# Performance work log

Hardware: AMD Instinct MI355X
Metric: run time of the kernel (lower is better)

## Reference

```python
import jax, jax.numpy as jnp
import numpy as np


def _hardswish(x):
    return x * jnp.clip(x + 3.0, 0.0, 6.0) / 6.0


def _rel_coords_table(W):
    # [1, 2W-1, 2W-1, 2], log-spaced continuous relative coords (SwinV2)
    rc = jnp.arange(-(W - 1), W, dtype=jnp.float32)
    grid = jnp.stack(jnp.meshgrid(rc, rc, indexing='ij'), axis=-1)[None]
    grid = grid / float(W - 1) * 8.0
    return jnp.sign(grid) * jnp.log2(jnp.abs(grid) + 1.0) / np.float32(np.log2(8.0))


def _rel_pos_index(W):
    # [N, N] int indices into the (2W-1)^2 bias table
    coords = np.stack(np.meshgrid(np.arange(W), np.arange(W), indexing='ij')).reshape(2, -1)
    rel = (coords[:, :, None] - coords[:, None, :]).transpose(1, 2, 0)  # [N, N, 2]
    rel[:, :, 0] += W - 1
    rel[:, :, 1] += W - 1
    rel[:, :, 0] *= 2 * W - 1
    return jnp.asarray(rel.sum(-1))


def setup_inputs() -> dict:
    key = jax.random.key(0)
    ks = jax.random.split(key, 6)
    dim, num_heads, W = 512, 16, 8
    N = W * W
    B, nW = 2048, 64
    return {
        'x': jax.random.normal(ks[0], (B, N, dim), jnp.float32),
        'mask': jax.random.normal(ks[1], (nW, N, N), jnp.float32),
        'w_qkv': jax.random.normal(ks[2], (dim, 3 * dim), jnp.float32) * 0.02,
        'w_out': jax.random.normal(ks[3], (dim, dim), jnp.float32) * 0.02,
        'cpb_w1': jax.random.normal(ks[4], (2, 512), jnp.float32) * 0.02,
        'cpb_w2': jax.random.normal(ks[5], (512, num_heads), jnp.float32) * 0.02,
        'logits_scale': jnp.log(10.0 * jnp.ones((num_heads, 1, 1), jnp.float32)),
        'window_size': W,
        'num_heads': num_heads,
    }


def reference(x, mask, w_qkv, w_out, cpb_w1, cpb_w2, logits_scale, window_size, num_heads):
    B, N, C = x.shape
    hd = C // num_heads
    qkv = (x @ w_qkv).reshape(B, N, 3, num_heads, hd).transpose(2, 0, 3, 1, 4)
    q, k, v = qkv[0], qkv[1], qkv[2]  # [B, H, N, hd]

    # cosine attention (L2-normalized q, k) with clamped learned logit scale
    qn = q / jnp.clip(jnp.linalg.norm(q, axis=-1, keepdims=True), 1e-12)
    kn = k / jnp.clip(jnp.linalg.norm(k, axis=-1, keepdims=True), 1e-12)
    attn = jnp.einsum('bhnd,bhmd->bhnm', qn, kn)
    scale = jnp.exp(jnp.minimum(logits_scale, jnp.log(jnp.float32(100.0))))  # [H,1,1]
    attn = attn * scale[None]

    # continuous position bias via tiny MLP + index gather, sigmoid-scaled
    table = _rel_coords_table(window_size)                       # [1, 2W-1, 2W-1, 2]
    bias_table = (_hardswish(table @ cpb_w1) @ cpb_w2).reshape(-1, num_heads)
    idx = _rel_pos_index(window_size)                            # [N, N]
    bias = bias_table[idx.reshape(-1)].reshape(N, N, num_heads).transpose(2, 0, 1)
    attn = attn + 16.0 * jax.nn.sigmoid(bias)[None]

    if mask is not None:
        nW = mask.shape[0]
        attn = attn.reshape(B // nW, nW, num_heads, N, N) + mask[None, :, None]
        attn = attn.reshape(B, num_heads, N, N)

    # NOTE: original uses nn.Softmax(1) -> softmax over the HEAD axis; replicate faithfully
    attn = jax.nn.softmax(attn, axis=1)

    out = jnp.einsum('bhnm,bhmd->bhnd', attn, v).transpose(0, 2, 1, 3).reshape(B, N, C)
    return out @ w_out
```

## Files before the change

kernel.cpp:

```cpp
#include <hip/hip_runtime.h>
#include <hip/hip_bf16.h>

typedef unsigned short u16;
typedef unsigned int u32;
typedef __attribute__((ext_vector_type(8))) short bf16x8;
typedef __attribute__((ext_vector_type(4))) short bf16x4;
typedef __attribute__((ext_vector_type(4))) float f32x4;
typedef __attribute__((ext_vector_type(4))) float float4v;

__device__ __forceinline__ float bf2f(u16 v) {
  union { u32 u; float f; } x; x.u = ((u32)v) << 16; return x.f;
}
__device__ __forceinline__ u16 f2bf(float f) {
  union { u32 u; float f; } x; x.f = f;
  return (u16)((x.u + 0x7fffu + ((x.u >> 16) & 1u)) >> 16);
}

__device__ __forceinline__ void gload16(const void* g, void* l) {
  __builtin_amdgcn_global_load_lds(
      (const __attribute__((address_space(1))) u32*)g,
      (__attribute__((address_space(3))) u32*)l, 16, 0, 0);
}

#define MFMA16(a, bfr, cacc) __builtin_amdgcn_mfma_f32_16x16x32_bf16((a), (bfr), (cacc), 0, 0, 0)

constexpr int KDIM = 512;


__global__ void convert_bf16_kernel(const float* __restrict__ in,
                                    u16* __restrict__ out, int n8) {
  int t = blockIdx.x * blockDim.x + threadIdx.x;
  if (t >= n8) return;
  const float4v* p = (const float4v*)(in + (size_t)t * 8);
  float4v a = p[0], b = p[1];
  union { bf16x8 v; u16 s[8]; } o;
  o.s[0] = f2bf(a[0]); o.s[1] = f2bf(a[1]); o.s[2] = f2bf(a[2]); o.s[3] = f2bf(a[3]);
  o.s[4] = f2bf(b[0]); o.s[5] = f2bf(b[1]); o.s[6] = f2bf(b[2]); o.s[7] = f2bf(b[3]);
  *(bf16x8*)(out + (size_t)t * 8) = o.v;
}

__global__ void transpose_kernel(const float* __restrict__ in, u16* __restrict__ out,
                                 int R, int C) {
  int t = blockIdx.x * blockDim.x + threadIdx.x;
  if (t >= R * C) return;
  int c = t / R, r = t % R;
  out[t] = f2bf(in[r * C + c]);
}

__global__ void mask_t_kernel(const float* __restrict__ in, float* __restrict__ out) {
  int t = blockIdx.x * blockDim.x + threadIdx.x;
  if (t >= 64 * 4096) return;
  int wm = t >> 12, rest = t & 4095, m = rest >> 6, n = rest & 63;
  out[t] = in[wm * 4096 + n * 64 + m];
}

__global__ void bias_tab_kernel(const float* __restrict__ w1, const float* __restrict__ w2,
                                float* __restrict__ tab) {
  int t = blockIdx.x * blockDim.x + threadIdx.x;
  if (t >= 225 * 16) return;
  int r = t >> 4, h = t & 15;
  int i = r / 15, j = r % 15;
  float gi = (float)(i - 7) * (8.0f / 7.0f);
  float gj = (float)(j - 7) * (8.0f / 7.0f);
  float si = (gi > 0.f) ? 1.f : ((gi < 0.f) ? -1.f : 0.f);
  float sj = (gj > 0.f) ? 1.f : ((gj < 0.f) ? -1.f : 0.f);
  float t0 = si * log2f(fabsf(gi) + 1.0f) * (1.0f / 3.0f);
  float t1 = sj * log2f(fabsf(gj) + 1.0f) * (1.0f / 3.0f);
  float acc = 0.f;
  for (int k = 0; k < 512; ++k) {
    float a = t0 * w1[k] + t1 * w1[512 + k];
    float hs = a * fminf(fmaxf(a + 3.f, 0.f), 6.f) * (1.f / 6.f);
    acc += hs * w2[k * 16 + h];
  }
  tab[t] = acc;
}

__global__ void bias16_kernel(const float* __restrict__ tab, float* __restrict__ b16) {
  int t = blockIdx.x * blockDim.x + threadIdx.x;
  if (t >= 16 * 64 * 64) return;
  int h = t >> 12, nm = t & 4095, m = nm >> 6, n = nm & 63;
  int idx = ((n >> 3) - (m >> 3) + 7) * 15 + ((n & 7) - (m & 7) + 7);
  float b = tab[idx * 16 + h];
  b16[t] = 16.0f / (1.0f + expf(-b));
}

template <bool F32OUT>
__global__ __launch_bounds__(256) void gemm_bt(const u16* __restrict__ A,
                                               const u16* __restrict__ Bt,
                                               void* __restrict__ Cout,
                                               int M, int N) {
  __shared__ u16 lA[128 * 64];
  __shared__ u16 lB[128 * 64];
  const int tid = threadIdx.x;
  const int w = tid >> 6, l = tid & 63;
  const int lg = l >> 4, li = l & 15;
  const int nbn = N >> 7;
  const int nwg = gridDim.x;
  int bidx = blockIdx.x;
  int q = nwg >> 3, r = nwg & 7;
  int xcd = bidx & 7, pos = bidx >> 3;
  int swz = (xcd < r ? xcd * (q + 1) : r * (q + 1) + (xcd - r) * q) + pos;
  int bm = swz / nbn, bn = swz % nbn;
  const int wr = w >> 1, wc = w & 1;

  f32x4 acc[4][4];
#pragma unroll
  for (int i = 0; i < 4; i++)
#pragma unroll
    for (int j = 0; j < 4; j++) acc[i][j] = (f32x4){0.f, 0.f, 0.f, 0.f};

  const u16* Abase = A + (size_t)(bm * 128) * KDIM;
  const u16* Bbase = Bt + (size_t)(bn * 128) * KDIM;

#pragma unroll
  for (int k0 = 0; k0 < KDIM; k0 += 64) {
#pragma unroll
    for (int i = 0; i < 4; ++i) {
      int c = w * 256 + i * 64 + l;
      int row = c >> 3, kc = c & 7;
      int kcs = kc ^ (row & 7);
      gload16(Abase + (size_t)row * KDIM + k0 + kcs * 8, (u16*)lA + c * 8);
      gload16(Bbase + (size_t)row * KDIM + k0 + kcs * 8, (u16*)lB + c * 8);
    }
    __syncthreads();
#pragma unroll
    for (int kk = 0; kk < 2; ++kk) {
      bf16x8 af[4], bfr[4];
#pragma unroll
      for (int t = 0; t < 4; ++t) {
        int row = wr * 64 + t * 16 + li;
        af[t] = *(const bf16x8*)&lA[row * 64 + (((kk * 4 + lg) ^ (row & 7)) << 3)];
        int col = wc * 64 + t * 16 + li;
        bfr[t] = *(const bf16x8*)&lB[col * 64 + (((kk * 4 + lg) ^ (col & 7)) << 3)];
      }
#pragma unroll
      for (int tm = 0; tm < 4; ++tm)
#pragma unroll
        for (int tn = 0; tn < 4; ++tn)
          acc[tm][tn] = MFMA16(af[tm], bfr[tn], acc[tm][tn]);
    }
    __syncthreads();
  }
  int r0 = bm * 128 + wr * 64 + lg * 4;
  int c0 = bn * 128 + wc * 64 + li;
#pragma unroll
  for (int tm = 0; tm < 4; ++tm)
#pragma unroll
    for (int tn = 0; tn < 4; ++tn)
#pragma unroll
      for (int j = 0; j < 4; ++j) {
        size_t off = (size_t)(r0 + tm * 16 + j) * N + c0 + tn * 16;
        if (F32OUT)
          ((float*)Cout)[off] = acc[tm][tn][j];
        else
          ((u16*)Cout)[off] = f2bf(acc[tm][tn][j]);
      }
}

__global__ __launch_bounds__(256) void gemm_qk(const u16* __restrict__ A,
                                               const u16* __restrict__ Bt,
                                               u16* __restrict__ Cq,
                                               const float* __restrict__ lscale) {
  __shared__ u16 lds[128 * 136];
  u16* lA = lds;
  u16* lB = lds + 8192;
  const int tid = threadIdx.x;
  const int w = tid >> 6, l = tid & 63;
  const int lg = l >> 4, li = l & 15;
  const int nbn = 8;
  const int nwg = gridDim.x;
  int bidx = blockIdx.x;
  int q = nwg >> 3, r = nwg & 7;
  int xcd = bidx & 7, pos = bidx >> 3;
  int swz = (xcd < r ? xcd * (q + 1) : r * (q + 1) + (xcd - r) * q) + pos;
  int bm = swz / nbn, bn = swz % nbn;
  const int wr = w >> 1, wc = w & 1;

  f32x4 acc[4][4];
#pragma unroll
  for (int i = 0; i < 4; i++)
#pragma unroll
    for (int j = 0; j < 4; j++) acc[i][j] = (f32x4){0.f, 0.f, 0.f, 0.f};

  const u16* Abase = A + (size_t)(bm * 128) * KDIM;
  const u16* Bbase = Bt + (size_t)(bn * 128) * KDIM;

#pragma unroll
  for (int k0 = 0; k0 < KDIM; k0 += 64) {
#pragma unroll
    for (int i = 0; i < 4; ++i) {
      int c = w * 256 + i * 64 + l;
      int row = c >> 3, kc = c & 7;
      int kcs = kc ^ (row & 7);
      gload16(Abase + (size_t)row * KDIM + k0 + kcs * 8, lA + c * 8);
      gload16(Bbase + (size_t)row * KDIM + k0 + kcs * 8, lB + c * 8);
    }
    __syncthreads();
#pragma unroll
    for (int kk = 0; kk < 2; ++kk) {
      bf16x8 af[4], bfr[4];
#pragma unroll
      for (int t = 0; t < 4; ++t) {
        int row = wr * 64 + t * 16 + li;
        af[t] = *(const bf16x8*)&lA[row * 64 + (((kk * 4 + lg) ^ (row & 7)) << 3)];
        int col = wc * 64 + t * 16 + li;
        bfr[t] = *(const bf16x8*)&lB[col * 64 + (((kk * 4 + lg) ^ (col & 7)) << 3)];
      }
#pragma unroll
      for (int tm = 0; tm < 4; ++tm)
#pragma unroll
        for (int tn = 0; tn < 4; ++tn)
          acc[tm][tn] = MFMA16(af[tm], bfr[tn], acc[tm][tn]);
    }
    __syncthreads();
  }

  const int s_t = bn >> 2;
  const int hq = (bn & 3) * 4;
  float scv[2];
  if (s_t == 0) {
    scv[0] = __expf(fminf(lscale[hq + wc * 2 + 0], 4.6051702f));
    scv[1] = __expf(fminf(lscale[hq + wc * 2 + 1], 4.6051702f));
  } else {
    scv[0] = scv[1] = 1.0f;
  }
#pragma unroll
  for (int tm = 0; tm < 4; ++tm)
#pragma unroll
    for (int g = 0; g < 2; ++g) {
      f32x4 s2;
#pragma unroll
      for (int j = 0; j < 4; ++j)
        s2[j] = acc[tm][2 * g][j] * acc[tm][2 * g][j] +
                acc[tm][2 * g + 1][j] * acc[tm][2 * g + 1][j];
#pragma unroll
      for (int m = 1; m <= 8; m <<= 1)
#pragma unroll
        for (int j = 0; j < 4; ++j) s2[j] += __shfl_xor(s2[j], m);
#pragma unroll
      for (int j = 0; j < 4; ++j) {
        float rn = scv[g] / fmaxf(sqrtf(s2[j]), 1e-12f);
        acc[tm][2 * g][j] *= rn;
        acc[tm][2 * g + 1][j] *= rn;
      }
    }
  u16* ct = lds;
#pragma unroll
  for (int tm = 0; tm < 4; ++tm)
#pragma unroll
    for (int tn = 0; tn < 4; ++tn)
#pragma unroll
      for (int j = 0; j < 4; ++j)
        ct[(wr * 64 + tm * 16 + lg * 4 + j) * 136 + wc * 64 + tn * 16 + li] =
            f2bf(acc[tm][tn][j]);
  __syncthreads();
  {
    int rr = tid >> 2;
    int c8 = (tid & 3) * 8;
#pragma unroll
    for (int bh = 0; bh < 2; ++bh)
#pragma unroll
      for (int ht = 0; ht < 4; ++ht) {
        bf16x8 v = *(const bf16x8*)(ct + (bh * 64 + rr) * 136 + ht * 32 + c8);
        size_t base = ((size_t)(s_t * 16 + hq + ht) * 2048 + (bm * 2 + bh)) * 2048;
        *(bf16x8*)(Cq + base + rr * 32 + c8) = v;
      }
  }
}

__global__ __launch_bounds__(256) void gemm_v(const u16* __restrict__ A,
                                              const u16* __restrict__ Bt,
                                              u16* __restrict__ Cq) {
  __shared__ u16 lds[128 * 136];
  u16* lA = lds;
  u16* lB = lds + 8192;
  const int tid = threadIdx.x;
  const int w = tid >> 6, l = tid & 63;
  const int lg = l >> 4, li = l & 15;
  const int nbn = 4;
  const int nwg = gridDim.x;
  int bidx = blockIdx.x;
  int q = nwg >> 3, r = nwg & 7;
  int xcd = bidx & 7, pos = bidx >> 3;
  int swz = (xcd < r ? xcd * (q + 1) : r * (q + 1) + (xcd - r) * q) + pos;
  int bm = swz / nbn, bn = swz % nbn;
  const int wr = w >> 1, wc = w & 1;

  f32x4 acc[4][4];
#pragma unroll
  for (int i = 0; i < 4; i++)
#pragma unroll
    for (int j = 0; j < 4; j++) acc[i][j] = (f32x4){0.f, 0.f, 0.f, 0.f};

  const u16* Abase = A + (size_t)(bm * 128) * KDIM;
  const u16* Bbase = Bt + (size_t)(bn * 128) * KDIM;

#pragma unroll
  for (int k0 = 0; k0 < KDIM; k0 += 64) {
#pragma unroll
    for (int i = 0; i < 4; ++i) {
      int c = w * 256 + i * 64 + l;
      int row = c >> 3, kc = c & 7;
      int kcs = kc ^ (row & 7);
      gload16(Abase + (size_t)row * KDIM + k0 + kcs * 8, lA + c * 8);
      gload16(Bbase + (size_t)row * KDIM + k0 + kcs * 8, lB + c * 8);
    }
    __syncthreads();
#pragma unroll
    for (int kk = 0; kk < 2; ++kk) {
      bf16x8 af[4], bfr[4];
#pragma unroll
      for (int t = 0; t < 4; ++t) {
        int row = wr * 64 + t * 16 + li;
        af[t] = *(const bf16x8*)&lA[row * 64 + (((kk * 4 + lg) ^ (row & 7)) << 3)];
        int col = wc * 64 + t * 16 + li;
        bfr[t] = *(const bf16x8*)&lB[col * 64 + (((kk * 4 + lg) ^ (col & 7)) << 3)];
      }
#pragma unroll
      for (int tm = 0; tm < 4; ++tm)
#pragma unroll
        for (int tn = 0; tn < 4; ++tn)
          acc[tm][tn] = MFMA16(af[tm], bfr[tn], acc[tm][tn]);
    }
    __syncthreads();
  }

  const int hq = bn * 4;
  u16* ctT = lds;
#pragma unroll
  for (int tm = 0; tm < 4; ++tm)
#pragma unroll
    for (int tn = 0; tn < 4; ++tn)
#pragma unroll
      for (int j = 0; j < 4; ++j)
        ctT[(wc * 64 + tn * 16 + li) * 136 + wr * 64 + tm * 16 + lg * 4 + j] =
            f2bf(acc[tm][tn][j]);
  __syncthreads();
#pragma unroll
  for (int r2 = 0; r2 < 8; ++r2) {
    int id = r2 * 256 + tid;
    int colc = id >> 4;
    int seg = id & 15;
    bf16x8 v = *(const bf16x8*)&ctT[colc * 136 + seg * 8];
    int ht = colc >> 5, d = colc & 31;
    int wi = seg >> 3, n0 = (seg & 7) * 8;
    size_t base = ((size_t)(32 + hq + ht) * 2048 + (bm * 2 + wi)) * 2048;
    *(bf16x8*)(Cq + base + d * 64 + n0) = v;
  }
}

__global__ __launch_bounds__(512, 2) void attn2(const u16* __restrict__ qkv,
                                                const float* __restrict__ maskT,
                                                const float* __restrict__ bias16T,
                                                u16* __restrict__ aout) {
  __shared__ float S[16 * 1088];
  u16* P16r = (u16*)S;
  float* ob = S;
  const int tid = threadIdx.x;
  const int w = tid >> 6, l = tid & 63;
  const int lg = l >> 4, li = l & 15;
  const int b = blockIdx.x, wm = b & 63;
  const float* maskT_w = maskT + wm * 4096;

  bf16x8 qfr[2][4];
#pragma unroll
  for (int hp = 0; hp < 2; ++hp) {
    const u16* qb = qkv + ((size_t)(w + hp * 8) * 2048 + b) * 2048;
#pragma unroll
    for (int tn = 0; tn < 4; ++tn)
      qfr[hp][tn] = *(const bf16x8*)(qb + (tn * 16 + li) * 32 + lg * 8);
  }

  f32x4 oacc[2][4][2];
#pragma unroll
  for (int hp = 0; hp < 2; ++hp)
#pragma unroll
    for (int i = 0; i < 4; ++i) {
      oacc[hp][i][0] = (f32x4){0.f, 0.f, 0.f, 0.f};
      oacc[hp][i][1] = (f32x4){0.f, 0.f, 0.f, 0.f};
    }

#pragma unroll
  for (int c = 0; c < 4; ++c) {
#pragma unroll
    for (int hp = 0; hp < 2; ++hp) {
      int h = w + hp * 8;
      const u16* kb = qkv + ((size_t)(16 + h) * 2048 + b) * 2048;
      const float* biasT_h = bias16T + h * 4096;
      bf16x8 kfc = *(const bf16x8*)(kb + (c * 16 + li) * 32 + lg * 8);
      int mg = c * 16 + li;
#pragma unroll
      for (int tn = 0; tn < 4; ++tn) {
        f32x4 z = {0.f, 0.f, 0.f, 0.f};
        f32x4 s = MFMA16(qfr[hp][tn], kfc, z);
        float4v b4 = *(const float4v*)(biasT_h + mg * 64 + tn * 16 + lg * 4);
        float4v m4 = *(const float4v*)(maskT_w + mg * 64 + tn * 16 + lg * 4);
        *(float4v*)&S[h * 1088 + li * 68 + tn * 16 + lg * 4] = s + b4 + m4;
      }
    }
    __syncthreads();
    float vals[2][16];
    float inv[2];
#pragma unroll
    for (int pp = 0; pp < 2; ++pp) {
      int p = tid + pp * 512;
      int base = (p >> 6) * 68 + (p & 63);
      float mx = -3.0e38f;
#pragma unroll
      for (int hh = 0; hh < 16; ++hh) {
        vals[pp][hh] = S[hh * 1088 + base];
        mx = fmaxf(mx, vals[pp][hh]);
      }
      float sum = 0.f;
#pragma unroll
      for (int hh = 0; hh < 16; ++hh) {
        float e = __expf(vals[pp][hh] - mx);
        vals[pp][hh] = e;
        sum += e;
      }
      inv[pp] = 1.0f / sum;
    }
    __syncthreads();
#pragma unroll
    for (int pp = 0; pp < 2; ++pp) {
      int p = tid + pp * 512;
      int m = p >> 6, n = p & 63;
#pragma unroll
      for (int hh = 0; hh < 16; ++hh)
        P16r[hh * 1280 + n * 20 + m] = f2bf(vals[pp][hh] * inv[pp]);
    }
    __syncthreads();
#pragma unroll
    for (int hp = 0; hp < 2; ++hp) {
      int h = w + hp * 8;
      const u16* vbT = qkv + ((size_t)(32 + h) * 2048 + b) * 2048;
      bf16x8 vf[2];
      if (lg < 2) {
#pragma unroll
        for (int td = 0; td < 2; ++td)
          vf[td] = *(const bf16x8*)(vbT + (td * 16 + li) * 64 + c * 16 + lg * 8);
      } else {
#pragma unroll
        for (int td = 0; td < 2; ++td)
#pragma unroll
          for (int e = 0; e < 8; ++e) vf[td][e] = 0;
      }
#pragma unroll
      for (int tn = 0; tn < 4; ++tn) {
        bf16x8 pf;
        if (lg < 2) {
          const u16* pb = P16r + h * 1280 + (tn * 16 + li) * 20 + lg * 8;
          bf16x4 plo = *(const bf16x4*)pb;
          bf16x4 phi = *(const bf16x4*)(pb + 4);
          pf[0] = plo[0]; pf[1] = plo[1]; pf[2] = plo[2]; pf[3] = plo[3];
          pf[4] = phi[0]; pf[5] = phi[1]; pf[6] = phi[2]; pf[7] = phi[3];
        } else {
#pragma unroll
          for (int e = 0; e < 8; ++e) pf[e] = 0;
        }
        oacc[hp][tn][0] = MFMA16(pf, vf[0], oacc[hp][tn][0]);
        oacc[hp][tn][1] = MFMA16(pf, vf[1], oacc[hp][tn][1]);
      }
    }
    __syncthreads();
  }

#pragma unroll
  for (int tn = 0; tn < 4; ++tn) {
#pragma unroll
    for (int hp = 0; hp < 2; ++hp) {
      int h = w + hp * 8;
#pragma unroll
      for (int td = 0; td < 2; ++td)
#pragma unroll
        for (int j = 0; j < 4; ++j)
          ob[(lg * 4 + j) * 516 + h * 32 + td * 16 + li] = oacc[hp][tn][td][j];
    }
    __syncthreads();
    {
      int rr = tid >> 5, c16 = (tid & 31) * 16;
      const float* src = ob + rr * 516 + c16;
      u16* dst = aout + ((size_t)b * 64 + tn * 16 + rr) * 512 + c16;
#pragma unroll
      for (int half = 0; half < 2; ++half) {
        union { bf16x8 v; u16 u[8]; } o;
#pragma unroll
        for (int e = 0; e < 8; ++e) o.u[e] = f2bf(src[half * 8 + e]);
        *(bf16x8*)(dst + half * 8) = o.v;
      }
    }
    __syncthreads();
  }
}

extern "C" void kernel_launch(void* const* d_in, const int* in_sizes, int n_in,
                              void* d_out, int out_size, void* d_ws, size_t ws_size,
                              hipStream_t stream) {
  const float* x = (const float*)d_in[0];
  const float* mask = (const float*)d_in[1];
  const float* w_qkv = (const float*)d_in[2];
  const float* w_out = (const float*)d_in[3];
  const float* cpb_w1 = (const float*)d_in[4];
  const float* cpb_w2 = (const float*)d_in[5];
  const float* lscale = (const float*)d_in[6];
  float* out = (float*)d_out;

  char* ws = (char*)d_ws;
  u16* wqkvT = (u16*)ws;
  u16* woutT = (u16*)(ws + 1572864ull);
  float* btab = (float*)(ws + 2097152ull);
  float* b16 = (float*)(ws + 2113536ull);
  float* maskT = (float*)(ws + 2375680ull);
  u16* qkv_ws = (u16*)(ws + 19152896ull);
  u16* xb = (u16*)(ws + 19152896ull + 402653184ull);
  u16* attn_out = xb;

  transpose_kernel<<<(512 * 1536 + 255) / 256, 256, 0, stream>>>(w_qkv, wqkvT, 512, 1536);
  transpose_kernel<<<(512 * 512 + 255) / 256, 256, 0, stream>>>(w_out, woutT, 512, 512);
  bias_tab_kernel<<<(225 * 16 + 255) / 256, 256, 0, stream>>>(cpb_w1, cpb_w2, btab);
  bias16_kernel<<<(16 * 64 * 64 + 255) / 256, 256, 0, stream>>>(btab, b16);
  mask_t_kernel<<<(64 * 4096 + 255) / 256, 256, 0, stream>>>(mask, maskT);

  convert_bf16_kernel<<<(131072 * 64 + 255) / 256, 256, 0, stream>>>(x, xb, 131072 * 64);

  gemm_qk<<<8192, 256, 0, stream>>>(xb, wqkvT, qkv_ws, lscale);
  gemm_v<<<4096, 256, 0, stream>>>(xb, wqkvT + (size_t)1024 * 512, qkv_ws);

  attn2<<<2048, 512, 0, stream>>>(qkv_ws, maskT, b16, attn_out);

  gemm_bt<true><<<4096, 256, 0, stream>>>(attn_out, woutT, out, 131072, 512);
}
```

Measured before the change: 849.2 us.

## Process key chunks in pairs to fill full K=32 MFMA in attention PV

The attention kernel now computes softmax for two 16-key chunks into a separate, larger bf16 P buffer before each PV step. The PV MFMA then uses the full 32-wide K dimension instead of zero-padding half the lanes, halving PV MFMA count and removing the lg<2 branches. The output epilogue converts to bf16 in LDS once and writes rows with vector stores, dropping the per-tile sync loop. The extra 80KB of shared memory for P may lower occupancy against the launch bound of 2 blocks.

```diff
diff --git a/kernel.cpp b/kernel.cpp
--- a/kernel.cpp
+++ b/kernel.cpp
@@ -354,8 +354,8 @@
                                                 const float* __restrict__ bias16T,
                                                 u16* __restrict__ aout) {
   __shared__ float S[16 * 1088];
-  u16* P16r = (u16*)S;
-  float* ob = S;
+  __shared__ __align__(16) u16 P16r[16 * 2560];
+  u16* o16 = (u16*)S;
   const int tid = threadIdx.x;
   const int w = tid >> 6, l = tid & 63;
   const int lg = l >> 4, li = l & 15;
@@ -381,83 +381,65 @@
     }
 
 #pragma unroll
-  for (int c = 0; c < 4; ++c) {
-#pragma unroll
-    for (int hp = 0; hp < 2; ++hp) {
-      int h = w + hp * 8;
-      const u16* kb = qkv + ((size_t)(16 + h) * 2048 + b) * 2048;
-      const float* biasT_h = bias16T + h * 4096;
-      bf16x8 kfc = *(const bf16x8*)(kb + (c * 16 + li) * 32 + lg * 8);
-      int mg = c * 16 + li;
-#pragma unroll
-      for (int tn = 0; tn < 4; ++tn) {
-        f32x4 z = {0.f, 0.f, 0.f, 0.f};
-        f32x4 s = MFMA16(qfr[hp][tn], kfc, z);
-        float4v b4 = *(const float4v*)(biasT_h + mg * 64 + tn * 16 + lg * 4);
-        float4v m4 = *(const float4v*)(maskT_w + mg * 64 + tn * 16 + lg * 4);
-        *(float4v*)&S[h * 1088 + li * 68 + tn * 16 + lg * 4] = s + b4 + m4;
-      }
-    }
-    __syncthreads();
-    float vals[2][16];
-    float inv[2];
-#pragma unroll
-    for (int pp = 0; pp < 2; ++pp) {
-      int p = tid + pp * 512;
-      int base = (p >> 6) * 68 + (p & 63);
-      float mx = -3.0e38f;
-#pragma unroll
-      for (int hh = 0; hh < 16; ++hh) {
-        vals[pp][hh] = S[hh * 1088 + base];
-        mx = fmaxf(mx, vals[pp][hh]);
-      }
-      float sum = 0.f;
-#pragma unroll
-      for (int hh = 0; hh < 16; ++hh) {
-        float e = __expf(vals[pp][hh] - mx);
-        vals[pp][hh] = e;
-        sum += e;
-      }
-      inv[pp] = 1.0f / sum;
-    }
-    __syncthreads();
-#pragma unroll
-    for (int pp = 0; pp < 2; ++pp) {
-      int p = tid + pp * 512;
-      int m = p >> 6, n = p & 63;
-#pragma unroll
-      for (int hh = 0; hh < 16; ++hh)
-        P16r[hh * 1280 + n * 20 + m] = f2bf(vals[pp][hh] * inv[pp]);
-    }
-    __syncthreads();
+  for (int c2 = 0; c2 < 2; ++c2) {
+#pragma unroll
+    for (int half = 0; half < 2; ++half) {
+      const int c = c2 * 2 + half;
+#pragma unroll
+      for (int hp = 0; hp < 2; ++hp) {
+        int h = w + hp * 8;
+        const u16* kb = qkv + ((size_t)(16 + h) * 2048 + b) * 2048;
+        const float* biasT_h = bias16T + h * 4096;
+        bf16x8 kfc = *(const bf16x8*)(kb + (c * 16 + li) * 32 + lg * 8);
+        int mg = c * 16 + li;
+#pragma unroll
+        for (int tn = 0; tn < 4; ++tn) {
+          f32x4 z = {0.f, 0.f, 0.f, 0.f};
+          f32x4 s = MFMA16(qfr[hp][tn], kfc, z);
+          float4v b4 = *(const float4v*)(biasT_h + mg * 64 + tn * 16 + lg * 4);
+          float4v m4 = *(const float4v*)(maskT_w + mg * 64 + tn * 16 + lg * 4);
+          *(float4v*)&S[h * 1088 + li * 68 + tn * 16 + lg * 4] = s + b4 + m4;
+        }
+      }
+      __syncthreads();
+#pragma unroll
+      for (int pp = 0; pp < 2; ++pp) {
+        int p = tid + pp * 512;
+        int m = p >> 6, n = p & 63;
+        int base = m * 68 + n;
+        float vals[16];
+        float mx = -3.0e38f;
+#pragma unroll
+        for (int hh = 0; hh < 16; ++hh) {
+          vals[hh] = S[hh * 1088 + base];
+          mx = fmaxf(mx, vals[hh]);
+        }
+        float sum = 0.f;
+#pragma unroll
+        for (int hh = 0; hh < 16; ++hh) {
+          float e = __expf(vals[hh] - mx);
+          vals[hh] = e;
+          sum += e;
+        }
+        float inv = 1.0f / sum;
+        int slot = half * 16 + m;
+#pragma unroll
+        for (int hh = 0; hh < 16; ++hh)
+          P16r[hh * 2560 + n * 40 + slot] = f2bf(vals[hh] * inv);
+      }
+      __syncthreads();
+    }
 #pragma unroll
     for (int hp = 0; hp < 2; ++hp) {
       int h = w + hp * 8;
       const u16* vbT = qkv + ((size_t)(32 + h) * 2048 + b) * 2048;
       bf16x8 vf[2];
-      if (lg < 2) {
-#pragma unroll
-        for (int td = 0; td < 2; ++td)
-          vf[td] = *(const bf16x8*)(vbT + (td * 16 + li) * 64 + c * 16 + lg * 8);
-      } else {
-#pragma unroll
-        for (int td = 0; td < 2; ++td)
-#pragma unroll
-          for (int e = 0; e < 8; ++e) vf[td][e] = 0;
-      }
+#pragma unroll
+      for (int td = 0; td < 2; ++td)
+        vf[td] = *(const bf16x8*)(vbT + (td * 16 + li) * 64 + c2 * 32 + lg * 8);
 #pragma unroll
       for (int tn = 0; tn < 4; ++tn) {
-        bf16x8 pf;
-        if (lg < 2) {
-          const u16* pb = P16r + h * 1280 + (tn * 16 + li) * 20 + lg * 8;
-          bf16x4 plo = *(const bf16x4*)pb;
-          bf16x4 phi = *(const bf16x4*)(pb + 4);
-          pf[0] = plo[0]; pf[1] = plo[1]; pf[2] = plo[2]; pf[3] = plo[3];
-          pf[4] = phi[0]; pf[5] = phi[1]; pf[6] = phi[2]; pf[7] = phi[3];
-        } else {
-#pragma unroll
-          for (int e = 0; e < 8; ++e) pf[e] = 0;
-        }
+        bf16x8 pf = *(const bf16x8*)&P16r[h * 2560 + (tn * 16 + li) * 40 + lg * 8];
         oacc[hp][tn][0] = MFMA16(pf, vf[0], oacc[hp][tn][0]);
         oacc[hp][tn][1] = MFMA16(pf, vf[1], oacc[hp][tn][1]);
       }
@@ -466,7 +448,7 @@
   }
 
 #pragma unroll
-  for (int tn = 0; tn < 4; ++tn) {
+  for (int tn = 0; tn < 4; ++tn)
 #pragma unroll
     for (int hp = 0; hp < 2; ++hp) {
       int h = w + hp * 8;
@@ -474,22 +456,19 @@
       for (int td = 0; td < 2; ++td)
 #pragma unroll
         for (int j = 0; j < 4; ++j)
-          ob[(lg * 4 + j) * 516 + h * 32 + td * 16 + li] = oacc[hp][tn][td][j];
-    }
-    __syncthreads();
-    {
-      int rr = tid >> 5, c16 = (tid & 31) * 16;
-      const float* src = ob + rr * 516 + c16;
-      u16* dst = aout + ((size_t)b * 64 + tn * 16 + rr) * 512 + c16;
-#pragma unroll
-      for (int half = 0; half < 2; ++half) {
-        union { bf16x8 v; u16 u[8]; } o;
-#pragma unroll
-        for (int e = 0; e < 8; ++e) o.u[e] = f2bf(src[half * 8 + e]);
-        *(bf16x8*)(dst + half * 8) = o.v;
-      }
-    }
-    __syncthreads();
+          o16[(tn * 16 + lg * 4 + j) * 528 + h * 32 + td * 16 + li] =
+              f2bf(oacc[hp][tn][td][j]);
+    }
+  __syncthreads();
+  {
+    int row = tid >> 3, seg = tid & 7;
+    u16* dst = aout + ((size_t)b * 64 + row) * 512;
+    const u16* src = o16 + row * 528;
+#pragma unroll
+    for (int i = 0; i < 8; ++i) {
+      int cc = (i * 8 + seg) * 8;
+      *(bf16x8*)(dst + cc) = *(const bf16x8*)(src + cc);
+    }
   }
 }
 
```

Result: faster. 813.1 us (-4.3%).
